# Kernel optimization log

Measured on AMD Instinct MI355X. Metric: run time of the kernel, lower is better.

Reference implementation:

```python
import jax, jax.numpy as jnp
import numpy as np

B, S = 4, 2048
IN_F, OUT_F = 4096, 4096
BLK = 8
NB_IN = IN_F // BLK   # 512
NB_OUT = OUT_F // BLK  # 512


def setup_inputs() -> dict:
    key = jax.random.key(0)
    k_x, k_c = jax.random.split(key)
    x = jax.random.normal(k_x, (B, S, IN_F), dtype=jnp.float32)
    # mimic xavier_uniform on (NB_OUT*NB_IN, BLK) then / sqrt(BLK)
    bound = float(np.sqrt(6.0 / (NB_OUT * NB_IN + BLK)))
    circ_params = jax.random.uniform(k_c, (NB_OUT, NB_IN, BLK), dtype=jnp.float32,
                                     minval=-bound, maxval=bound) / np.sqrt(BLK)
    bias = jnp.zeros((OUT_F,), dtype=jnp.float32)
    return {"x": x, "circ_params": circ_params, "bias": bias}


def reference(x, circ_params, bias):
    # x: (B, S, IN_F) -> (B, S, NB_IN, BLK)
    xb = x.reshape(*x.shape[:-1], NB_IN, BLK)
    x_rfft = jnp.fft.rfft(xb, axis=-1)              # (B, S, NB_IN, BLK//2+1) complex
    c_rfft = jnp.fft.rfft(circ_params, axis=-1)     # (NB_OUT, NB_IN, BLK//2+1) complex
    # per-frequency block contraction: sum over input blocks i
    out_rfft = jnp.einsum('bsif,nif->bsnf', x_rfft, c_rfft)  # (B, S, NB_OUT, BLK//2+1)
    out = jnp.fft.irfft(out_rfft, n=BLK, axis=-1)   # (B, S, NB_OUT, BLK)
    out = out.reshape(*x.shape[:-1], OUT_F)
    return out + bias
```

## Files before the change

### kernel.cpp

```cpp
#include <hip/hip_runtime.h>

#define AS1 __attribute__((address_space(1)))
#define AS3 __attribute__((address_space(3)))

typedef __attribute__((ext_vector_type(8))) short short8;
typedef __attribute__((ext_vector_type(4))) float floatx4;
typedef __attribute__((ext_vector_type(8))) unsigned short u16x8;
typedef __attribute__((ext_vector_type(4))) unsigned short u16x4;
typedef __attribute__((ext_vector_type(4))) float f32x4;

#define M_DIM 8192
#define K_DIM 4096
#define N_DIM 4096
#define NB    512

#define SQ2H 0.70710678118654752f

#define P0_OFF 0
#define P1_OFF 4194304
#define P2_OFF 12582912
#define P3_OFF 20971520
#define P4_OFF 29360128
#define Q0_OFF 0
#define Q1_OFF 262144
#define Q2_OFF 1310720
#define Q3_OFF 2359296
#define Q4_OFF 3407872

static __device__ __forceinline__ unsigned short f32_to_bf16(float f) {
  union { float f; unsigned int u; } v;
  v.f = f;
  return (unsigned short)((v.u + 0x7FFFu + ((v.u >> 16) & 1u)) >> 16);
}
static __device__ __forceinline__ float bf16_to_f32(unsigned short h) {
  union { unsigned int u; float f; } v;
  v.u = ((unsigned int)h) << 16;
  return v.f;
}

struct F8 { float a0, a4, r1, i1, r2, i2, r3, i3; };
static __device__ __forceinline__ F8 rfft8(const float* x) {
  F8 o;
  o.a0 = x[0]+x[1]+x[2]+x[3]+x[4]+x[5]+x[6]+x[7];
  o.a4 = x[0]-x[1]+x[2]-x[3]+x[4]-x[5]+x[6]-x[7];
  const float d1 = x[1]-x[3]-x[5]+x[7];
  const float s1 = x[1]+x[3]-x[5]-x[7];
  o.r1 = x[0]-x[4] + SQ2H*d1;
  o.i1 = -(SQ2H*s1 + x[2]-x[6]);
  o.r2 = x[0]-x[2]+x[4]-x[6];
  o.i2 = -(x[1]-x[3]+x[5]-x[7]);
  o.r3 = x[0]-x[4] - SQ2H*d1;
  o.i3 = -(SQ2H*s1 - x[2]+x[6]);
  return o;
}


__global__ __launch_bounds__(256) void xtransform_kernel(
    const float* __restrict__ x, unsigned short* __restrict__ XF)
{
  const int tid = blockIdx.x * 256 + threadIdx.x;
  const int m = tid >> 9;
  const int i = tid & 511;
  float v[8];
  *reinterpret_cast<f32x4*>(v)     = *reinterpret_cast<const f32x4*>(x + (size_t)tid * 8);
  *reinterpret_cast<f32x4*>(v + 4) = *reinterpret_cast<const f32x4*>(x + (size_t)tid * 8 + 4);
  F8 f = rfft8(v);
  XF[P0_OFF + (size_t)m * 512 + i] = f32_to_bf16(f.a0);
  XF[P4_OFF + (size_t)m * 512 + i] = f32_to_bf16(f.a4);
  unsigned int p1 = (unsigned int)f32_to_bf16(f.r1) | ((unsigned int)f32_to_bf16(f.i1) << 16);
  unsigned int p2 = (unsigned int)f32_to_bf16(f.r2) | ((unsigned int)f32_to_bf16(f.i2) << 16);
  unsigned int p3 = (unsigned int)f32_to_bf16(f.r3) | ((unsigned int)f32_to_bf16(f.i3) << 16);
  *reinterpret_cast<unsigned int*>(XF + P1_OFF + (size_t)m * 1024 + 2 * i) = p1;
  *reinterpret_cast<unsigned int*>(XF + P2_OFF + (size_t)m * 1024 + 2 * i) = p2;
  *reinterpret_cast<unsigned int*>(XF + P3_OFF + (size_t)m * 1024 + 2 * i) = p3;
}

__global__ __launch_bounds__(256) void wtransform_kernel(
    const float* __restrict__ c, unsigned short* __restrict__ WF)
{
  const int tid = blockIdx.x * 256 + threadIdx.x;
  const int n = tid >> 9;
  const int i = tid & 511;
  float v[8];
  *reinterpret_cast<f32x4*>(v)     = *reinterpret_cast<const f32x4*>(c + (size_t)tid * 8);
  *reinterpret_cast<f32x4*>(v + 4) = *reinterpret_cast<const f32x4*>(c + (size_t)tid * 8 + 4);
  F8 f = rfft8(v);
  WF[Q0_OFF + (size_t)n * 512 + i] = f32_to_bf16(f.a0);
  WF[Q4_OFF + (size_t)n * 512 + i] = f32_to_bf16(f.a4);
  unsigned int q1or = (unsigned int)f32_to_bf16(f.r1) | ((unsigned int)f32_to_bf16(-f.i1) << 16);
  unsigned int q1oi = (unsigned int)f32_to_bf16(f.i1) | ((unsigned int)f32_to_bf16(f.r1) << 16);
  unsigned int q2or = (unsigned int)f32_to_bf16(f.r2) | ((unsigned int)f32_to_bf16(-f.i2) << 16);
  unsigned int q2oi = (unsigned int)f32_to_bf16(f.i2) | ((unsigned int)f32_to_bf16(f.r2) << 16);
  unsigned int q3or = (unsigned int)f32_to_bf16(f.r3) | ((unsigned int)f32_to_bf16(-f.i3) << 16);
  unsigned int q3oi = (unsigned int)f32_to_bf16(f.i3) | ((unsigned int)f32_to_bf16(f.r3) << 16);
  *reinterpret_cast<unsigned int*>(WF + Q1_OFF + (size_t)n * 1024 + 2 * i)         = q1or;
  *reinterpret_cast<unsigned int*>(WF + Q1_OFF + (size_t)(512 + n) * 1024 + 2 * i) = q1oi;
  *reinterpret_cast<unsigned int*>(WF + Q2_OFF + (size_t)n * 1024 + 2 * i)         = q2or;
  *reinterpret_cast<unsigned int*>(WF + Q2_OFF + (size_t)(512 + n) * 1024 + 2 * i) = q2oi;
  *reinterpret_cast<unsigned int*>(WF + Q3_OFF + (size_t)n * 1024 + 2 * i)         = q3or;
  *reinterpret_cast<unsigned int*>(WF + Q3_OFF + (size_t)(512 + n) * 1024 + 2 * i) = q3oi;
}

__global__ __launch_bounds__(256) void gemm_freq_kernel(
    const unsigned short* __restrict__ XF,
    const unsigned short* __restrict__ WF,
    unsigned short* __restrict__ OF)
{
  int K, aoff, boff;
  switch (blockIdx.z) {
    case 0:  K = 512;  aoff = P0_OFF; boff = Q0_OFF; break;
    case 1:  K = 1024; aoff = P1_OFF; boff = Q1_OFF; break;
    case 2:  K = 1024; aoff = P2_OFF; boff = Q2_OFF; break;
    case 3:  K = 1024; aoff = P3_OFF; boff = Q3_OFF; break;
    default: K = 512;  aoff = P4_OFF; boff = Q4_OFF; break;
  }
  const int n0 = blockIdx.x * 128;
  if (n0 >= K) return;
  const int m0 = blockIdx.y * 128;

  const unsigned short* A  = XF + aoff;
  const unsigned short* Bm = WF + boff;
  unsigned short* C        = OF + aoff;

  __shared__ alignas(16) unsigned short As[128 * 32];
  __shared__ alignas(16) unsigned short Bs[128 * 32];

  const int tid  = threadIdx.x;
  const int lane = tid & 63;
  const int wave = tid >> 6;
  const int wm   = wave >> 1;
  const int wn   = wave & 1;
  const int quad = lane >> 4;
  const int l15  = lane & 15;

  floatx4 acc[4][4];
#pragma unroll
  for (int i = 0; i < 4; ++i)
#pragma unroll
    for (int j = 0; j < 4; ++j) acc[i][j] = (floatx4){0.f, 0.f, 0.f, 0.f};

  for (int k0 = 0; k0 < K; k0 += 32) {
#pragma unroll
    for (int j = 0; j < 2; ++j) {
      const int chunk = j * 256 + wave * 64 + lane;
      const int row   = chunk >> 2;
      const int kc    = (chunk & 3) << 3;
      const unsigned short* ga = A  + (size_t)(m0 + row) * K + (k0 + kc);
      const unsigned short* gb = Bm + (size_t)(n0 + row) * K + (k0 + kc);
      unsigned short* la = As + (j * 256 + wave * 64) * 8;
      unsigned short* lb = Bs + (j * 256 + wave * 64) * 8;
      __builtin_amdgcn_global_load_lds((AS1 void*)ga, (AS3 void*)la, 16, 0, 0);
      __builtin_amdgcn_global_load_lds((AS1 void*)gb, (AS3 void*)lb, 16, 0, 0);
    }
    __syncthreads();

    short8 af[4], bf[4];
#pragma unroll
    for (int mi = 0; mi < 4; ++mi)
      af[mi] = *reinterpret_cast<const short8*>(As + (wm * 64 + mi * 16 + l15) * 32 + quad * 8);
#pragma unroll
    for (int ni = 0; ni < 4; ++ni)
      bf[ni] = *reinterpret_cast<const short8*>(Bs + (wn * 64 + ni * 16 + l15) * 32 + quad * 8);

#pragma unroll
    for (int mi = 0; mi < 4; ++mi)
#pragma unroll
      for (int ni = 0; ni < 4; ++ni)
        acc[mi][ni] = __builtin_amdgcn_mfma_f32_16x16x32_bf16(
            af[mi], bf[ni], acc[mi][ni], 0, 0, 0);
    __syncthreads();
  }

#pragma unroll
  for (int mi = 0; mi < 4; ++mi) {
#pragma unroll
    for (int r = 0; r < 4; ++r) {
      const int grow = m0 + wm * 64 + mi * 16 + quad * 4 + r;
      unsigned short* crow = C + (size_t)grow * K;
#pragma unroll
      for (int ni = 0; ni < 4; ++ni)
        crow[n0 + wn * 64 + ni * 16 + l15] = f32_to_bf16(acc[mi][ni][r]);
    }
  }
}

__global__ __launch_bounds__(256) void irfft_kernel(
    const unsigned short* __restrict__ OF,
    const float* __restrict__ bias,
    float* __restrict__ out)
{
  const int tid = blockIdx.x * 256 + threadIdx.x;
  const int m   = tid >> 7;
  const int nb4 = tid & 127;

  const u16x4 a0v = *reinterpret_cast<const u16x4*>(OF + P0_OFF + (size_t)m * 512 + nb4 * 4);
  const u16x4 a4v = *reinterpret_cast<const u16x4*>(OF + P4_OFF + (size_t)m * 512 + nb4 * 4);
  const u16x4 r1v = *reinterpret_cast<const u16x4*>(OF + P1_OFF + (size_t)m * 1024 + nb4 * 4);
  const u16x4 i1v = *reinterpret_cast<const u16x4*>(OF + P1_OFF + (size_t)m * 1024 + 512 + nb4 * 4);
  const u16x4 r2v = *reinterpret_cast<const u16x4*>(OF + P2_OFF + (size_t)m * 1024 + nb4 * 4);
  const u16x4 i2v = *reinterpret_cast<const u16x4*>(OF + P2_OFF + (size_t)m * 1024 + 512 + nb4 * 4);
  const u16x4 r3v = *reinterpret_cast<const u16x4*>(OF + P3_OFF + (size_t)m * 1024 + nb4 * 4);
  const u16x4 i3v = *reinterpret_cast<const u16x4*>(OF + P3_OFF + (size_t)m * 1024 + 512 + nb4 * 4);

#pragma unroll
  for (int j = 0; j < 4; ++j) {
    const int nblk = nb4 * 4 + j;
    const float a0 = bf16_to_f32(a0v[j]), a4 = bf16_to_f32(a4v[j]);
    const float r1 = bf16_to_f32(r1v[j]), i1 = bf16_to_f32(i1v[j]);
    const float r2 = bf16_to_f32(r2v[j]), i2 = bf16_to_f32(i2v[j]);
    const float r3 = bf16_to_f32(r3v[j]), i3 = bf16_to_f32(i3v[j]);

    const float ep = a0 + a4, em = a0 - a4;
    const float sr1 = SQ2H * r1, si1 = SQ2H * i1;
    const float sr3 = SQ2H * r3, si3 = SQ2H * i3;
    float o[8];
    o[0] = (ep + 2.f * ( r1 + r2 + r3)) * 0.125f;
    o[1] = (em + 2.f * ( sr1 - si1 - i2 - sr3 - si3)) * 0.125f;
    o[2] = (ep + 2.f * (-i1 - r2 + i3)) * 0.125f;
    o[3] = (em + 2.f * (-sr1 - si1 + i2 + sr3 - si3)) * 0.125f;
    o[4] = (ep + 2.f * (-r1 + r2 - r3)) * 0.125f;
    o[5] = (em + 2.f * (-sr1 + si1 - i2 + sr3 + si3)) * 0.125f;
    o[6] = (ep + 2.f * ( i1 - r2 - i3)) * 0.125f;
    o[7] = (em + 2.f * ( sr1 + si1 + i2 - sr3 + si3)) * 0.125f;

    const float* bs = bias + nblk * 8;
    f32x4 lo, hi;
#pragma unroll
    for (int t = 0; t < 4; ++t) { lo[t] = o[t] + bs[t]; hi[t] = o[t + 4] + bs[t + 4]; }
    float* dst = out + (size_t)m * N_DIM + nblk * 8;
    *reinterpret_cast<f32x4*>(dst)     = lo;
    *reinterpret_cast<f32x4*>(dst + 4) = hi;
  }
}


__global__ __launch_bounds__(256) void convert_x_kernel(
    const float* __restrict__ x, unsigned short* __restrict__ Xb)
{
  const size_t t = (size_t)blockIdx.x * 256 + threadIdx.x;
  const f32x4 a = *reinterpret_cast<const f32x4*>(x + t * 8);
  const f32x4 b = *reinterpret_cast<const f32x4*>(x + t * 8 + 4);
  union { u16x8 v; unsigned short s[8]; } o;
#pragma unroll
  for (int u = 0; u < 4; ++u) { o.s[u] = f32_to_bf16(a[u]); o.s[u + 4] = f32_to_bf16(b[u]); }
  *reinterpret_cast<u16x8*>(Xb + t * 8) = o.v;
}

__global__ __launch_bounds__(256) void expand_w_kernel(
    const float* __restrict__ c, unsigned short* __restrict__ W)
{
  const int tid = blockIdx.x * 256 + threadIdx.x;
  const int o = tid >> 9, i = tid & 511, n = o >> 3, t = o & 7;
  const float* src = c + ((size_t)(n * NB + i) << 3);
  float raw[8];
  *reinterpret_cast<f32x4*>(raw)     = *reinterpret_cast<const f32x4*>(src);
  *reinterpret_cast<f32x4*>(raw + 4) = *reinterpret_cast<const f32x4*>(src + 4);
  union { u16x8 v; unsigned short s[8]; } outv;
#pragma unroll
  for (int u = 0; u < 8; ++u) outv.s[u] = f32_to_bf16(raw[(t - u) & 7]);
  *reinterpret_cast<u16x8*>(W + (size_t)o * K_DIM + i * 8) = outv.v;
}

__global__ __launch_bounds__(256) void gemm_bt_kernel(
    const unsigned short* __restrict__ A, const unsigned short* __restrict__ Bm,
    const float* __restrict__ bias, float* __restrict__ C)
{
  __shared__ alignas(16) unsigned short As[128 * 32];
  __shared__ alignas(16) unsigned short Bs[128 * 32];
  const int tid = threadIdx.x, lane = tid & 63, wave = tid >> 6;
  const int wm = wave >> 1, wn = wave & 1;
  const int m0 = blockIdx.y * 128, n0 = blockIdx.x * 128;
  const int quad = lane >> 4, l15 = lane & 15;

  floatx4 acc[4][4];
#pragma unroll
  for (int i = 0; i < 4; ++i)
#pragma unroll
    for (int j = 0; j < 4; ++j) acc[i][j] = (floatx4){0.f, 0.f, 0.f, 0.f};

  for (int k0 = 0; k0 < K_DIM; k0 += 32) {
#pragma unroll
    for (int j = 0; j < 2; ++j) {
      const int chunk = j * 256 + wave * 64 + lane;
      const int row = chunk >> 2, kc = (chunk & 3) << 3;
      const unsigned short* ga = A  + (size_t)(m0 + row) * K_DIM + (k0 + kc);
      const unsigned short* gb = Bm + (size_t)(n0 + row) * K_DIM + (k0 + kc);
      unsigned short* la = As + (j * 256 + wave * 64) * 8;
      unsigned short* lb = Bs + (j * 256 + wave * 64) * 8;
      __builtin_amdgcn_global_load_lds((AS1 void*)ga, (AS3 void*)la, 16, 0, 0);
      __builtin_amdgcn_global_load_lds((AS1 void*)gb, (AS3 void*)lb, 16, 0, 0);
    }
    __syncthreads();
    short8 af[4], bf[4];
#pragma unroll
    for (int mi = 0; mi < 4; ++mi)
      af[mi] = *reinterpret_cast<const short8*>(As + (wm * 64 + mi * 16 + l15) * 32 + quad * 8);
#pragma unroll
    for (int ni = 0; ni < 4; ++ni)
      bf[ni] = *reinterpret_cast<const short8*>(Bs + (wn * 64 + ni * 16 + l15) * 32 + quad * 8);
#pragma unroll
    for (int mi = 0; mi < 4; ++mi)
#pragma unroll
      for (int ni = 0; ni < 4; ++ni)
        acc[mi][ni] = __builtin_amdgcn_mfma_f32_16x16x32_bf16(af[mi], bf[ni], acc[mi][ni], 0, 0, 0);
    __syncthreads();
  }
  float bv[4]; int cols[4];
#pragma unroll
  for (int ni = 0; ni < 4; ++ni) { cols[ni] = n0 + wn * 64 + ni * 16 + l15; bv[ni] = bias[cols[ni]]; }
#pragma unroll
  for (int mi = 0; mi < 4; ++mi)
#pragma unroll
    for (int r = 0; r < 4; ++r) {
      const int grow = m0 + wm * 64 + mi * 16 + quad * 4 + r;
      float* crow = C + (size_t)grow * N_DIM;
#pragma unroll
      for (int ni = 0; ni < 4; ++ni) crow[cols[ni]] = acc[mi][ni][r] + bv[ni];
    }
}

extern "C" void kernel_launch(void* const* d_in, const int* in_sizes, int n_in,
                              void* d_out, int out_size, void* d_ws, size_t ws_size,
                              hipStream_t stream) {
  const float* x    = (const float*)d_in[0];
  const float* circ = (const float*)d_in[1];
  const float* bias = (const float*)d_in[2];
  float* out = (float*)d_out;

  const size_t XF_BYTES = (size_t)33554432 * 2;
  const size_t WF_BYTES = (size_t)3670016 * 2;
  const size_t OF_BYTES = (size_t)33554432 * 2;
  const size_t NEED = XF_BYTES + WF_BYTES + OF_BYTES;

  if (ws_size >= NEED) {
    unsigned short* XF = (unsigned short*)d_ws;
    unsigned short* WF = (unsigned short*)((char*)d_ws + XF_BYTES);
    unsigned short* OF = (unsigned short*)((char*)d_ws + XF_BYTES + WF_BYTES);

    wtransform_kernel<<<(NB * NB) / 256, 256, 0, stream>>>(circ, WF);
    xtransform_kernel<<<(M_DIM * NB) / 256, 256, 0, stream>>>(x, XF);
    dim3 grid(8, M_DIM / 128, 5);
    gemm_freq_kernel<<<grid, 256, 0, stream>>>(XF, WF, OF);
    irfft_kernel<<<(M_DIM * 128) / 256, 256, 0, stream>>>(OF, bias, out);
  } else {
    unsigned short* W  = (unsigned short*)d_ws;
    unsigned short* Xb = (unsigned short*)((char*)d_ws + (size_t)N_DIM * K_DIM * 2);
    convert_x_kernel<<<(M_DIM * K_DIM / 8) / 256, 256, 0, stream>>>(x, Xb);
    expand_w_kernel<<<(N_DIM * NB) / 256, 256, 0, stream>>>(circ, W);
    dim3 grid(N_DIM / 128, M_DIM / 128);
    gemm_bt_kernel<<<grid, 256, 0, stream>>>(Xb, W, bias, out);
  }
}
```

Measured before the change: 386.9 us.

## Vectorize FFT transform stores, compact GEMM grid with swizzle, stage irfft output via LDS

```diff
diff --git a/kernel.cpp b/kernel.cpp
--- a/kernel.cpp
+++ b/kernel.cpp
@@ -59,20 +59,30 @@
     const float* __restrict__ x, unsigned short* __restrict__ XF)
 {
   const int tid = blockIdx.x * 256 + threadIdx.x;
-  const int m = tid >> 9;
-  const int i = tid & 511;
-  float v[8];
-  *reinterpret_cast<f32x4*>(v)     = *reinterpret_cast<const f32x4*>(x + (size_t)tid * 8);
-  *reinterpret_cast<f32x4*>(v + 4) = *reinterpret_cast<const f32x4*>(x + (size_t)tid * 8 + 4);
-  F8 f = rfft8(v);
-  XF[P0_OFF + (size_t)m * 512 + i] = f32_to_bf16(f.a0);
-  XF[P4_OFF + (size_t)m * 512 + i] = f32_to_bf16(f.a4);
-  unsigned int p1 = (unsigned int)f32_to_bf16(f.r1) | ((unsigned int)f32_to_bf16(f.i1) << 16);
-  unsigned int p2 = (unsigned int)f32_to_bf16(f.r2) | ((unsigned int)f32_to_bf16(f.i2) << 16);
-  unsigned int p3 = (unsigned int)f32_to_bf16(f.r3) | ((unsigned int)f32_to_bf16(f.i3) << 16);
-  *reinterpret_cast<unsigned int*>(XF + P1_OFF + (size_t)m * 1024 + 2 * i) = p1;
-  *reinterpret_cast<unsigned int*>(XF + P2_OFF + (size_t)m * 1024 + 2 * i) = p2;
-  *reinterpret_cast<unsigned int*>(XF + P3_OFF + (size_t)m * 1024 + 2 * i) = p3;
+  const int m  = tid >> 7;
+  const int i4 = tid & 127;
+  float v[32];
+#pragma unroll
+  for (int q = 0; q < 8; ++q)
+    *reinterpret_cast<f32x4*>(v + q * 4) =
+        *reinterpret_cast<const f32x4*>(x + (size_t)m * 4096 + i4 * 32 + q * 4);
+
+  u16x4 p0, p4;
+  u16x8 p1, p2, p3;
+#pragma unroll
+  for (int g = 0; g < 4; ++g) {
+    F8 f = rfft8(v + g * 8);
+    p0[g] = f32_to_bf16(f.a0);
+    p4[g] = f32_to_bf16(f.a4);
+    p1[2*g] = f32_to_bf16(f.r1); p1[2*g+1] = f32_to_bf16(f.i1);
+    p2[2*g] = f32_to_bf16(f.r2); p2[2*g+1] = f32_to_bf16(f.i2);
+    p3[2*g] = f32_to_bf16(f.r3); p3[2*g+1] = f32_to_bf16(f.i3);
+  }
+  *reinterpret_cast<u16x4*>(XF + P0_OFF + (size_t)m * 512 + i4 * 4) = p0;
+  *reinterpret_cast<u16x4*>(XF + P4_OFF + (size_t)m * 512 + i4 * 4) = p4;
+  *reinterpret_cast<u16x8*>(XF + P1_OFF + (size_t)m * 1024 + i4 * 8) = p1;
+  *reinterpret_cast<u16x8*>(XF + P2_OFF + (size_t)m * 1024 + i4 * 8) = p2;
+  *reinterpret_cast<u16x8*>(XF + P3_OFF + (size_t)m * 1024 + i4 * 8) = p3;
 }
 
 __global__ __launch_bounds__(256) void wtransform_kernel(
@@ -106,17 +116,25 @@
     const unsigned short* __restrict__ WF,
     unsigned short* __restrict__ OF)
 {
+  const int bid = blockIdx.x;
+  const int swz = (bid & 7) * 256 + (bid >> 3);
+  const int mt  = swz >> 5;
+  const int yf  = swz & 31;
+  int z, nt;
+  if (yf < 4)       { z = 0; nt = yf; }
+  else if (yf < 28) { z = 1 + ((yf - 4) >> 3); nt = (yf - 4) & 7; }
+  else              { z = 4; nt = yf - 28; }
+
   int K, aoff, boff;
-  switch (blockIdx.z) {
+  switch (z) {
     case 0:  K = 512;  aoff = P0_OFF; boff = Q0_OFF; break;
     case 1:  K = 1024; aoff = P1_OFF; boff = Q1_OFF; break;
     case 2:  K = 1024; aoff = P2_OFF; boff = Q2_OFF; break;
     case 3:  K = 1024; aoff = P3_OFF; boff = Q3_OFF; break;
     default: K = 512;  aoff = P4_OFF; boff = Q4_OFF; break;
   }
-  const int n0 = blockIdx.x * 128;
-  if (n0 >= K) return;
-  const int m0 = blockIdx.y * 128;
+  const int n0 = nt * 128;
+  const int m0 = mt * 128;
 
   const unsigned short* A  = XF + aoff;
   const unsigned short* Bm = WF + boff;
@@ -189,9 +207,11 @@
     const float* __restrict__ bias,
     float* __restrict__ out)
 {
-  const int tid = blockIdx.x * 256 + threadIdx.x;
-  const int m   = tid >> 7;
-  const int nb4 = tid & 127;
+  __shared__ alignas(16) float lds[256 * 36];
+  const int t   = threadIdx.x;
+  const int gt  = blockIdx.x * 256 + t;
+  const int m   = gt >> 7;
+  const int nb4 = gt & 127;
 
   const u16x4 a0v = *reinterpret_cast<const u16x4*>(OF + P0_OFF + (size_t)m * 512 + nb4 * 4);
   const u16x4 a4v = *reinterpret_cast<const u16x4*>(OF + P4_OFF + (size_t)m * 512 + nb4 * 4);
@@ -202,6 +222,7 @@
   const u16x4 r3v = *reinterpret_cast<const u16x4*>(OF + P3_OFF + (size_t)m * 1024 + nb4 * 4);
   const u16x4 i3v = *reinterpret_cast<const u16x4*>(OF + P3_OFF + (size_t)m * 1024 + 512 + nb4 * 4);
 
+  float res[32];
 #pragma unroll
   for (int j = 0; j < 4; ++j) {
     const int nblk = nb4 * 4 + j;
@@ -223,13 +244,28 @@
     o[6] = (ep + 2.f * ( i1 - r2 - i3)) * 0.125f;
     o[7] = (em + 2.f * ( sr1 + si1 + i2 - sr3 + si3)) * 0.125f;
 
-    const float* bs = bias + nblk * 8;
-    f32x4 lo, hi;
-#pragma unroll
-    for (int t = 0; t < 4; ++t) { lo[t] = o[t] + bs[t]; hi[t] = o[t + 4] + bs[t + 4]; }
-    float* dst = out + (size_t)m * N_DIM + nblk * 8;
-    *reinterpret_cast<f32x4*>(dst)     = lo;
-    *reinterpret_cast<f32x4*>(dst + 4) = hi;
+    const f32x4 blo = *reinterpret_cast<const f32x4*>(bias + nblk * 8);
+    const f32x4 bhi = *reinterpret_cast<const f32x4*>(bias + nblk * 8 + 4);
+#pragma unroll
+    for (int k = 0; k < 4; ++k) {
+      res[j * 8 + k]     = o[k]     + blo[k];
+      res[j * 8 + 4 + k] = o[k + 4] + bhi[k];
+    }
+  }
+
+  float* dst = lds + t * 36;
+#pragma unroll
+  for (int p = 0; p < 8; ++p)
+    *reinterpret_cast<f32x4*>(dst + p * 4) = *reinterpret_cast<const f32x4*>(res + p * 4);
+  __syncthreads();
+
+  float* gbase = out + (size_t)blockIdx.x * 8192;
+#pragma unroll
+  for (int s = 0; s < 8; ++s) {
+    const int off16 = s * 256 + t;
+    const f32x4 vv = *reinterpret_cast<const f32x4*>(
+        lds + (off16 >> 3) * 36 + (off16 & 7) * 4);
+    *reinterpret_cast<f32x4*>(gbase + off16 * 4) = vv;
   }
 }
 
@@ -338,10 +374,9 @@
     unsigned short* OF = (unsigned short*)((char*)d_ws + XF_BYTES + WF_BYTES);
 
     wtransform_kernel<<<(NB * NB) / 256, 256, 0, stream>>>(circ, WF);
-    xtransform_kernel<<<(M_DIM * NB) / 256, 256, 0, stream>>>(x, XF);
-    dim3 grid(8, M_DIM / 128, 5);
-    gemm_freq_kernel<<<grid, 256, 0, stream>>>(XF, WF, OF);
-    irfft_kernel<<<(M_DIM * 128) / 256, 256, 0, stream>>>(OF, bias, out);
+    xtransform_kernel<<<(M_DIM * NB / 4) / 256, 256, 0, stream>>>(x, XF);
+    gemm_freq_kernel<<<2048, 256, 0, stream>>>(XF, WF, OF);
+    irfft_kernel<<<M_DIM / 2, 256, 0, stream>>>(OF, bias, out);
   } else {
     unsigned short* W  = (unsigned short*)d_ws;
     unsigned short* Xb = (unsigned short*)((char*)d_ws + (size_t)N_DIM * K_DIM * 2);
```

Measured after the change: 363.6 us. -6.0%, faster.
